# Kernel optimization log

Measured on AMD Instinct MI355X. Metric: run time of the kernel, lower is better.

Reference implementation:

```python
import jax, jax.numpy as jnp
import numpy as np

EMB = 384
H = 6
D = 64
B = 256
T = 256


def setup_inputs() -> dict:
    key = jax.random.key(0)
    ks = jax.random.split(key, 6)
    s = 1.0 / np.sqrt(EMB)
    return {
        "x": jax.random.normal(ks[0], (B, T, EMB), dtype=jnp.float32),
        "wq": jax.random.normal(ks[1], (H, EMB, D), dtype=jnp.float32) * s,
        "wk": jax.random.normal(ks[2], (H, EMB, D), dtype=jnp.float32) * s,
        "wv": jax.random.normal(ks[3], (H, EMB, D), dtype=jnp.float32) * s,
        "w_proj": jax.random.normal(ks[4], (H * D, EMB), dtype=jnp.float32) * s,
        "b_proj": jax.random.normal(ks[5], (EMB,), dtype=jnp.float32) * 0.01,
    }


def reference(x, wq, wk, wv, w_proj, b_proj):
    # x: [B, T, E]; per-head projections stacked over H (dropout in eval mode)
    q = jnp.einsum("bte,hed->bhtd", x, wq)
    k = jnp.einsum("bte,hed->bhtd", x, wk)
    v = jnp.einsum("bte,hed->bhtd", x, wv)
    scale = q.shape[-1] ** -0.5
    scores = jnp.einsum("bhqd,bhkd->bhqk", q, k) * scale  # [B,H,T,T]
    tq = q.shape[2]
    causal = jnp.tril(jnp.ones((tq, tq), dtype=bool))
    scores = jnp.where(causal, scores, -jnp.inf)
    att = jax.nn.softmax(scores, axis=-1)
    out = jnp.einsum("bhqk,bhkd->bhqd", att, v)  # [B,H,T,D]
    out = out.transpose(0, 2, 1, 3).reshape(x.shape[0], tq, -1)  # concat heads
    return out @ w_proj + b_proj
```

## Files before the change

kernel.cpp:

```cpp
#include <hip/hip_runtime.h>
#include <hip/hip_bf16.h>


#define Bn 256
#define Tn 256
#define En 384
#define Hn 6
#define Dn 64

typedef __bf16 bf16x8 __attribute__((ext_vector_type(8)));
typedef float f32x4 __attribute__((ext_vector_type(4)));
typedef unsigned short u16x8 __attribute__((ext_vector_type(8)));

static __device__ __forceinline__ unsigned short f2bf(float f) {
    unsigned int u = __builtin_bit_cast(unsigned int, f);
    u += 0x7fffu + ((u >> 16) & 1u);
    return (unsigned short)(u >> 16);
}

static __device__ __forceinline__ f32x4 mfma16(bf16x8 a, bf16x8 b, f32x4 c) {
    return __builtin_amdgcn_mfma_f32_16x16x32_bf16(a, b, c, 0, 0, 0);
}

static __device__ __forceinline__ void glds16(const unsigned short* g, unsigned short* l) {
    __builtin_amdgcn_global_load_lds(
        (const __attribute__((address_space(1))) unsigned int*)g,
        (__attribute__((address_space(3))) unsigned int*)l, 16, 0, 0);
}

__global__ __launch_bounds__(256) void prep_xcast_kernel(
    const float* __restrict__ wq, const float* __restrict__ wk,
    const float* __restrict__ wv, const float* __restrict__ wp,
    const float* __restrict__ x,
    unsigned short* __restrict__ wt, unsigned short* __restrict__ wpt,
    unsigned short* __restrict__ xb) {
    const int bid = blockIdx.x;
    if (bid < 12288) {
        size_t i = ((size_t)bid * 256 + threadIdx.x) * 8;
        float4 f0 = *(const float4*)(x + i);
        float4 f1 = *(const float4*)(x + i + 4);
        u16x8 p;
        p[0] = f2bf(f0.x); p[1] = f2bf(f0.y); p[2] = f2bf(f0.z); p[3] = f2bf(f0.w);
        p[4] = f2bf(f1.x); p[5] = f2bf(f1.y); p[6] = f2bf(f1.z); p[7] = f2bf(f1.w);
        *(u16x8*)(xb + i) = p;
    } else {
        const int NW = 3 * Hn * Dn * En;
        const int NP = En * En;
        int idx = (bid - 12288) * 256 + threadIdx.x;
        if (idx < NW) {
            int e = idx % En;
            int d = (idx / En) % Dn;
            int h = (idx / (En * Dn)) % Hn;
            int t = idx / (En * Dn * Hn);
            const float* src = (t == 0) ? wq : (t == 1) ? wk : wv;
            wt[idx] = f2bf(src[(h * En + e) * Dn + d]);
        } else if (idx < NW + NP) {
            int j = idx - NW;
            int k = j % En;
            int n = j / En;
            wpt[j] = f2bf(wp[k * En + n]);
        }
    }
}

__global__ __launch_bounds__(256) void qkv_gemm(
    const unsigned short* __restrict__ xb, const unsigned short* __restrict__ wt,
    unsigned short* __restrict__ Qo, unsigned short* __restrict__ Ko,
    unsigned short* __restrict__ Vt) {
    __shared__ unsigned short As[4][128][32];
    __shared__ unsigned short Bs[4][192][32];

    const int bid = blockIdx.x;
    const int swz = (bid & 7) * 384 + (bid >> 3);
    const int h = swz % Hn;
    const int m0 = (swz / Hn) * 128;

    const int tid = threadIdx.x;
    const int wave = tid >> 6, lane = tid & 63;
    const int quad = lane >> 4, l16 = lane & 15;
    const int mw = (wave >> 1) * 64, nw = (wave & 1) * 96;

    f32x4 acc[4][6];
#pragma unroll
    for (int i = 0; i < 4; ++i)
#pragma unroll
        for (int j = 0; j < 6; ++j) acc[i][j] = (f32x4){0.f, 0.f, 0.f, 0.f};

    const int lrow = lane >> 2;
    const int js = (lane & 3) ^ ((lane >> 3) & 3);

    const unsigned short* ga[2];
#pragma unroll
    for (int i = 0; i < 2; ++i)
        ga[i] = xb + (size_t)(m0 + wave * 32 + i * 16 + lrow) * En + js * 8;
    const unsigned short* gb[3];
#pragma unroll
    for (int i = 0; i < 3; ++i) {
        int n = wave * 48 + i * 16 + lrow;
        gb[i] = wt + (size_t)(((n >> 6) * Hn + h) * Dn + (n & 63)) * En + js * 8;
    }

#define QKV_STAGE(buf, koff)                                              \
    do {                                                                  \
        glds16(ga[0] + (koff), &As[buf][wave * 32][0]);                   \
        glds16(ga[1] + (koff), &As[buf][wave * 32 + 16][0]);              \
        glds16(gb[0] + (koff), &Bs[buf][wave * 48][0]);                   \
        glds16(gb[1] + (koff), &Bs[buf][wave * 48 + 16][0]);              \
        glds16(gb[2] + (koff), &Bs[buf][wave * 48 + 32][0]);              \
    } while (0)

    QKV_STAGE(0, 0);
    QKV_STAGE(1, 32);
    QKV_STAGE(2, 64);

    const int ps = (quad ^ ((l16 >> 1) & 3)) * 8;

#pragma unroll
    for (int kb = 0; kb < 12; ++kb) {
        if (kb <= 9)       asm volatile("s_waitcnt vmcnt(10)" ::: "memory");
        else if (kb == 10) asm volatile("s_waitcnt vmcnt(5)" ::: "memory");
        else               asm volatile("s_waitcnt vmcnt(0)" ::: "memory");
        __builtin_amdgcn_s_barrier();
        if (kb < 9) QKV_STAGE((kb + 3) & 3, (kb + 3) * 32);

        const int cur = kb & 3;
        bf16x8 a[4], b[6];
#pragma unroll
        for (int mi = 0; mi < 4; ++mi)
            a[mi] = *(const bf16x8*)&As[cur][mw + mi * 16 + l16][ps];
#pragma unroll
        for (int ni = 0; ni < 6; ++ni)
            b[ni] = *(const bf16x8*)&Bs[cur][nw + ni * 16 + l16][ps];
#pragma unroll
        for (int mi = 0; mi < 4; ++mi)
#pragma unroll
            for (int ni = 0; ni < 6; ++ni) acc[mi][ni] = mfma16(a[mi], b[ni], acc[mi][ni]);
    }
#undef QKV_STAGE

    const int b = m0 >> 8, tbase = m0 & 255;
    unsigned short* qkbase[2] = {
        Qo + (size_t)((b * Hn + h) * Tn) * Dn,
        Ko + (size_t)((b * Hn + h) * Tn) * Dn };
    unsigned short* vdst = Vt + (size_t)((b * Hn + h) * Dn) * Tn;
#pragma unroll
    for (int ni = 0; ni < 6; ++ni) {
        const int ng = nw + ni * 16;
        const int tensor = ng >> 6;
        const int d = (ng & 63) + l16;
        if (tensor < 2) {
            unsigned short* dst = qkbase[tensor];
#pragma unroll
            for (int mi = 0; mi < 4; ++mi)
#pragma unroll
                for (int r = 0; r < 4; ++r) {
                    int t = tbase + mw + mi * 16 + quad * 4 + r;
                    dst[t * Dn + d] = f2bf(acc[mi][ni][r]);
                }
        } else {
#pragma unroll
            for (int mi = 0; mi < 4; ++mi) {
                int t0 = tbase + mw + mi * 16 + quad * 4;
                ushort4 pk;
                pk.x = f2bf(acc[mi][ni][0]);
                pk.y = f2bf(acc[mi][ni][1]);
                pk.z = f2bf(acc[mi][ni][2]);
                pk.w = f2bf(acc[mi][ni][3]);
                *(ushort4*)&vdst[d * Tn + t0] = pk;
            }
        }
    }
}

__global__ __launch_bounds__(256) void attn_kernel(
    const unsigned short* __restrict__ Q, const unsigned short* __restrict__ K,
    const unsigned short* __restrict__ Vt, unsigned short* __restrict__ attout) {
    __shared__ unsigned short Kt[256][64];
    __shared__ unsigned short Vl[64][256];
    __shared__ unsigned short P[4][16][72];

    const int h = blockIdx.x, b = blockIdx.y;
    const unsigned short* Qb = Q + (size_t)((b * Hn + h) * Tn) * Dn;
    const unsigned short* Kb = K + (size_t)((b * Hn + h) * Tn) * Dn;
    const unsigned short* Vb = Vt + (size_t)((b * Hn + h) * Dn) * Tn;

    const int tid = threadIdx.x;
    const int wave = tid >> 6, lane = tid & 63;
    const int quad = lane >> 4, l16 = lane & 15;

    const int grp[4] = {wave, 7 - wave, 8 + wave, 15 - wave};

    {
        const unsigned short* kg = Kb + (size_t)(lane >> 3) * Dn + ((lane & 7) ^ (lane >> 3)) * 8;
#pragma unroll
        for (int i = 0; i < 8; ++i) {
            const int c = wave * 8 + i;
            glds16(kg + (size_t)c * 8 * Dn, &Kt[c * 8][0]);
        }
#pragma unroll
        for (int i = 0; i < 8; ++i) {
            const int c = wave * 8 + i;
            const int d = c * 2 + (lane >> 5);
            const int j = (lane & 31) ^ (d & 7);
            glds16(Vb + (size_t)d * Tn + j * 8, &Vl[c * 2][0]);
        }
    }

    bf16x8 aq[4][2];
#pragma unroll
    for (int gi = 0; gi < 4; ++gi) {
        const int q0 = grp[gi] * 16;
#pragma unroll
        for (int ks = 0; ks < 2; ++ks)
            aq[gi][ks] = *(const bf16x8*)&Qb[(q0 + l16) * Dn + ks * 32 + quad * 8];
    }

    __syncthreads();

    const float cexp = 0.125f * 1.44269504f;

#pragma unroll
    for (int gi = 0; gi < 4; ++gi) {
        const int g = grp[gi];
        const int q0 = g * 16;

        f32x4 O[4];
#pragma unroll
        for (int i = 0; i < 4; ++i) O[i] = (f32x4){0.f, 0.f, 0.f, 0.f};
        float rsum[4] = {0.f, 0.f, 0.f, 0.f};

        const int ktmax = g >> 2;
        for (int kt = 0; kt <= ktmax; ++kt) {
            f32x4 S[4];
#pragma unroll
            for (int i = 0; i < 4; ++i) S[i] = (f32x4){0.f, 0.f, 0.f, 0.f};
            __builtin_amdgcn_s_setprio(1);
#pragma unroll
            for (int ks = 0; ks < 2; ++ks)
#pragma unroll
                for (int ni = 0; ni < 4; ++ni) {
                    bf16x8 bk = *(const bf16x8*)
                        &Kt[kt * 64 + ni * 16 + l16][(((ks * 4 + quad) ^ (l16 & 7)) * 8)];
                    S[ni] = mfma16(aq[gi][ks], bk, S[ni]);
                }
            __builtin_amdgcn_s_setprio(0);

#pragma unroll
            for (int ni = 0; ni < 4; ++ni)
#pragma unroll
                for (int r = 0; r < 4; ++r) {
                    int col = kt * 64 + ni * 16 + l16;
                    float p = exp2f(S[ni][r] * cexp);
                    p = (col > q0 + quad * 4 + r) ? 0.f : p;
                    rsum[r] += p;
                    P[wave][quad * 4 + r][ni * 16 + l16] = f2bf(p);
                }

            __builtin_amdgcn_s_setprio(1);
#pragma unroll
            for (int ks = 0; ks < 2; ++ks) {
                bf16x8 ap = *(const bf16x8*)&P[wave][l16][ks * 32 + quad * 8];
#pragma unroll
                for (int ni = 0; ni < 4; ++ni) {
                    bf16x8 bv = *(const bf16x8*)
                        &Vl[ni * 16 + l16][(((kt * 8 + ks * 4 + quad) ^ (l16 & 7)) * 8)];
                    O[ni] = mfma16(ap, bv, O[ni]);
                }
            }
            __builtin_amdgcn_s_setprio(0);
        }

#pragma unroll
        for (int r = 0; r < 4; ++r) {
            float s = rsum[r];
            s += __shfl_xor(s, 1);
            s += __shfl_xor(s, 2);
            s += __shfl_xor(s, 4);
            s += __shfl_xor(s, 8);
            rsum[r] = s;
        }

#pragma unroll
        for (int r = 0; r < 4; ++r) {
            float inv = 1.0f / rsum[r];
#pragma unroll
            for (int ni = 0; ni < 4; ++ni)
                P[wave][quad * 4 + r][ni * 16 + l16] = f2bf(O[ni][r] * inv);
        }
        const int row = lane >> 2;
        const int colc = (lane & 3) * 16;
        unsigned short* dst = attout + (size_t)(b * Tn + q0 + row) * (Hn * Dn) + h * Dn + colc;
        *(uint4*)dst = *(const uint4*)&P[wave][row][colc];
        *(uint4*)(dst + 8) = *(const uint4*)&P[wave][row][colc + 8];
    }
}

__global__ __launch_bounds__(256) void proj_gemm(
    const unsigned short* __restrict__ attout, const unsigned short* __restrict__ wpt,
    const float* __restrict__ bproj, float* __restrict__ out) {
    __shared__ unsigned short As[2][128][64];
    __shared__ unsigned short Bs[2][128][64];

    const int bid = blockIdx.x;
    const int swz = (bid & 7) * 192 + (bid >> 3);
    const int n0 = (swz % 3) * 128;
    const int m0 = (swz / 3) * 128;

    const int tid = threadIdx.x;
    const int wave = tid >> 6, lane = tid & 63;
    const int quad = lane >> 4, l16 = lane & 15;
    const int mw = (wave >> 1) * 64, nw = (wave & 1) * 64;

    f32x4 acc[4][4];
#pragma unroll
    for (int i = 0; i < 4; ++i)
#pragma unroll
        for (int j = 0; j < 4; ++j) acc[i][j] = (f32x4){0.f, 0.f, 0.f, 0.f};

    const int lr = lane >> 3;
    const int js = (lane & 7) ^ lr;

    const unsigned short* ga[4];
    const unsigned short* gb[4];
#pragma unroll
    for (int i = 0; i < 4; ++i) {
        ga[i] = attout + (size_t)(m0 + wave * 32 + i * 8 + lr) * En + js * 8;
        gb[i] = wpt + (size_t)(n0 + wave * 32 + i * 8 + lr) * En + js * 8;
    }

#define PROJ_STAGE(buf, koff)                                             \
    do {                                                                  \
        _Pragma("unroll") for (int i = 0; i < 4; ++i)                     \
            glds16(ga[i] + (koff), &As[buf][wave * 32 + i * 8][0]);       \
        _Pragma("unroll") for (int i = 0; i < 4; ++i)                     \
            glds16(gb[i] + (koff), &Bs[buf][wave * 32 + i * 8][0]);       \
    } while (0)

    PROJ_STAGE(0, 0);
    PROJ_STAGE(1, 64);

#pragma unroll
    for (int kb = 0; kb < 6; ++kb) {
        if (kb < 5) asm volatile("s_waitcnt vmcnt(8)" ::: "memory");
        else        asm volatile("s_waitcnt vmcnt(0)" ::: "memory");
        __builtin_amdgcn_s_barrier();

        const int cur = kb & 1;
        __builtin_amdgcn_s_setprio(1);
#pragma unroll
        for (int ks = 0; ks < 2; ++ks) {
            bf16x8 a[4], bb[4];
            const int ps = ((ks * 4 + quad) ^ (l16 & 7)) * 8;
#pragma unroll
            for (int mi = 0; mi < 4; ++mi)
                a[mi] = *(const bf16x8*)&As[cur][mw + mi * 16 + l16][ps];
#pragma unroll
            for (int ni = 0; ni < 4; ++ni)
                bb[ni] = *(const bf16x8*)&Bs[cur][nw + ni * 16 + l16][ps];
#pragma unroll
            for (int mi = 0; mi < 4; ++mi)
#pragma unroll
                for (int ni = 0; ni < 4; ++ni) acc[mi][ni] = mfma16(a[mi], bb[ni], acc[mi][ni]);
        }
        __builtin_amdgcn_s_setprio(0);

        if (kb < 4) {
            __builtin_amdgcn_s_barrier();
            PROJ_STAGE(cur, (kb + 2) * 64);
        }
    }
#undef PROJ_STAGE

#pragma unroll
    for (int mi = 0; mi < 4; ++mi)
#pragma unroll
        for (int ni = 0; ni < 4; ++ni)
#pragma unroll
            for (int r = 0; r < 4; ++r) {
                int row = m0 + mw + mi * 16 + quad * 4 + r;
                int col = n0 + nw + ni * 16 + l16;
                out[(size_t)row * En + col] = acc[mi][ni][r] + bproj[col];
            }
}

extern "C" void kernel_launch(void* const* d_in, const int* in_sizes, int n_in,
                              void* d_out, int out_size, void* d_ws, size_t ws_size,
                              hipStream_t stream) {
    const float* x  = (const float*)d_in[0];
    const float* wq = (const float*)d_in[1];
    const float* wk = (const float*)d_in[2];
    const float* wv = (const float*)d_in[3];
    const float* wp = (const float*)d_in[4];
    const float* bp = (const float*)d_in[5];
    float* out = (float*)d_out;

    char* ws = (char*)d_ws;
    const size_t WT_OFF  = 0;
    const size_t WPT_OFF = WT_OFF + 884736;
    const size_t Q_OFF   = WPT_OFF + 294912;
    const size_t K_OFF   = Q_OFF + 50331648ull;
    const size_t VT_OFF  = K_OFF + 50331648ull;
    const size_t XB_OFF  = VT_OFF + 50331648ull;

    unsigned short* wt   = (unsigned short*)(ws + WT_OFF);
    unsigned short* wpt  = (unsigned short*)(ws + WPT_OFF);
    unsigned short* Qd   = (unsigned short*)(ws + Q_OFF);
    unsigned short* Kd   = (unsigned short*)(ws + K_OFF);
    unsigned short* Vtd  = (unsigned short*)(ws + VT_OFF);
    unsigned short* xbd  = (unsigned short*)(ws + XB_OFF);
    unsigned short* ao   = xbd;

    prep_xcast_kernel<<<14592, 256, 0, stream>>>(wq, wk, wv, wp, x, wt, wpt, xbd);
    qkv_gemm<<<3072, 256, 0, stream>>>(xbd, wt, Qd, Kd, Vtd);
    attn_kernel<<<dim3(Hn, Bn), 256, 0, stream>>>(Qd, Kd, Vtd, ao);
    proj_gemm<<<1536, 256, 0, stream>>>(ao, wpt, bp, out);
}
```

Baseline: 360.4 us.

## Fuse QKV projection GEMM into attention kernel, keeping Q/K/V in LDS

Merges the QKV GEMM and attention kernels so each block computes Q, K and V for one (batch, head) pair directly into shared memory and then runs causal attention on them. This removes the global-memory round trip for Q, K and V and one kernel launch. In exchange each block uses about 156KB of LDS, which limits occupancy to one block per CU, the grid shrinks, and the GEMM pipeline drops from four stages to three, so latency hiding is weaker.

```diff
diff --git a/kernel.cpp b/kernel.cpp
--- a/kernel.cpp
+++ b/kernel.cpp
@@ -63,17 +63,21 @@
     }
 }
 
-__global__ __launch_bounds__(256) void qkv_gemm(
+__global__ __launch_bounds__(256, 1) void qkvattn_kernel(
     const unsigned short* __restrict__ xb, const unsigned short* __restrict__ wt,
-    unsigned short* __restrict__ Qo, unsigned short* __restrict__ Ko,
-    unsigned short* __restrict__ Vt) {
-    __shared__ unsigned short As[4][128][32];
-    __shared__ unsigned short Bs[4][192][32];
+    unsigned short* __restrict__ attout) {
+    __shared__ __align__(16) unsigned short smem[79872];
+    unsigned short (*Kt)[64]      = (unsigned short(*)[64])(smem);
+    unsigned short (*Vl)[256]     = (unsigned short(*)[256])(smem + 16384);
+    unsigned short (*Qs)[64]      = (unsigned short(*)[64])(smem + 32768);
+    unsigned short (*As)[128][32] = (unsigned short(*)[128][32])(smem + 49152);
+    unsigned short (*Bs)[192][32] = (unsigned short(*)[192][32])(smem + 61440);
+    unsigned short (*P)[16][72]   = (unsigned short(*)[16][72])(smem + 49152);
 
     const int bid = blockIdx.x;
-    const int swz = (bid & 7) * 384 + (bid >> 3);
-    const int h = swz % Hn;
-    const int m0 = (swz / Hn) * 128;
+    const int swz = (bid & 7) * 192 + (bid >> 3);
+    const int bi = swz / Hn;
+    const int h  = swz % Hn;
 
     const int tid = threadIdx.x;
     const int wave = tid >> 6, lane = tid & 63;
@@ -92,7 +96,7 @@
     const unsigned short* ga[2];
 #pragma unroll
     for (int i = 0; i < 2; ++i)
-        ga[i] = xb + (size_t)(m0 + wave * 32 + i * 16 + lrow) * En + js * 8;
+        ga[i] = xb + (size_t)(bi * 256 + wave * 32 + i * 16 + lrow) * En + js * 8;
     const unsigned short* gb[3];
 #pragma unroll
     for (int i = 0; i < 3; ++i) {
@@ -100,130 +104,103 @@
         gb[i] = wt + (size_t)(((n >> 6) * Hn + h) * Dn + (n & 63)) * En + js * 8;
     }
 
-#define QKV_STAGE(buf, koff)                                              \
-    do {                                                                  \
-        glds16(ga[0] + (koff), &As[buf][wave * 32][0]);                   \
-        glds16(ga[1] + (koff), &As[buf][wave * 32 + 16][0]);              \
-        glds16(gb[0] + (koff), &Bs[buf][wave * 48][0]);                   \
-        glds16(gb[1] + (koff), &Bs[buf][wave * 48 + 16][0]);              \
-        glds16(gb[2] + (koff), &Bs[buf][wave * 48 + 32][0]);              \
+#define QA_STAGE(c)                                                          \
+    do {                                                                     \
+        const int _buf = (c) % 3;                                            \
+        const size_t _ao = (size_t)((c) / 12) * (128 * En) + ((c) % 12) * 32;\
+        const size_t _bo = (size_t)((c) % 12) * 32;                          \
+        glds16(ga[0] + _ao, &As[_buf][wave * 32][0]);                        \
+        glds16(ga[1] + _ao, &As[_buf][wave * 32 + 16][0]);                   \
+        glds16(gb[0] + _bo, &Bs[_buf][wave * 48][0]);                        \
+        glds16(gb[1] + _bo, &Bs[_buf][wave * 48 + 16][0]);                   \
+        glds16(gb[2] + _bo, &Bs[_buf][wave * 48 + 32][0]);                   \
     } while (0)
 
-    QKV_STAGE(0, 0);
-    QKV_STAGE(1, 32);
-    QKV_STAGE(2, 64);
+#define QA_EPI(half)                                                         \
+    do {                                                                     \
+        _Pragma("unroll") for (int ni = 0; ni < 6; ++ni) {                   \
+            const int ng = nw + ni * 16;                                     \
+            const int tensor = ng >> 6;                                      \
+            const int d = (ng & 63) + l16;                                   \
+            if (tensor == 2) {                                               \
+                _Pragma("unroll") for (int mi = 0; mi < 4; ++mi) {           \
+                    const int t0 = (half) * 128 + mw + mi * 16 + quad * 4;   \
+                    ushort4 pk;                                              \
+                    pk.x = f2bf(acc[mi][ni][0]);                             \
+                    pk.y = f2bf(acc[mi][ni][1]);                             \
+                    pk.z = f2bf(acc[mi][ni][2]);                             \
+                    pk.w = f2bf(acc[mi][ni][3]);                             \
+                    *(ushort4*)&Vl[d][((((t0 >> 3) ^ (d & 7))) << 3) + (t0 & 4)] = pk; \
+                }                                                            \
+            } else {                                                         \
+                unsigned short(*dstl)[64] = (tensor == 0) ? Qs : Kt;         \
+                _Pragma("unroll") for (int mi = 0; mi < 4; ++mi)             \
+                    _Pragma("unroll") for (int r = 0; r < 4; ++r) {          \
+                        const int t = (half) * 128 + mw + mi * 16 + quad * 4 + r; \
+                        dstl[t][((((d >> 3) ^ (t & 7))) << 3) + (d & 7)] =   \
+                            f2bf(acc[mi][ni][r]);                            \
+                    }                                                        \
+            }                                                                \
+        }                                                                    \
+    } while (0)
+
+    QA_STAGE(0);
+    QA_STAGE(1);
 
     const int ps = (quad ^ ((l16 >> 1) & 3)) * 8;
 
 #pragma unroll
-    for (int kb = 0; kb < 12; ++kb) {
-        if (kb <= 9)       asm volatile("s_waitcnt vmcnt(10)" ::: "memory");
-        else if (kb == 10) asm volatile("s_waitcnt vmcnt(5)" ::: "memory");
-        else               asm volatile("s_waitcnt vmcnt(0)" ::: "memory");
+    for (int k = 0; k < 24; ++k) {
         __builtin_amdgcn_s_barrier();
-        if (kb < 9) QKV_STAGE((kb + 3) & 3, (kb + 3) * 32);
-
-        const int cur = kb & 3;
-        bf16x8 a[4], b[6];
+        if (k < 22) {
+            QA_STAGE(k + 2);
+            asm volatile("s_waitcnt vmcnt(10)" ::: "memory");
+        } else if (k == 22) {
+            asm volatile("s_waitcnt vmcnt(5)" ::: "memory");
+        } else {
+            asm volatile("s_waitcnt vmcnt(0)" ::: "memory");
+        }
+
+        const int cur = k % 3;
+        bf16x8 a[4], bq[6];
 #pragma unroll
         for (int mi = 0; mi < 4; ++mi)
             a[mi] = *(const bf16x8*)&As[cur][mw + mi * 16 + l16][ps];
 #pragma unroll
         for (int ni = 0; ni < 6; ++ni)
-            b[ni] = *(const bf16x8*)&Bs[cur][nw + ni * 16 + l16][ps];
+            bq[ni] = *(const bf16x8*)&Bs[cur][nw + ni * 16 + l16][ps];
 #pragma unroll
         for (int mi = 0; mi < 4; ++mi)
 #pragma unroll
-            for (int ni = 0; ni < 6; ++ni) acc[mi][ni] = mfma16(a[mi], b[ni], acc[mi][ni]);
-    }
-#undef QKV_STAGE
-
-    const int b = m0 >> 8, tbase = m0 & 255;
-    unsigned short* qkbase[2] = {
-        Qo + (size_t)((b * Hn + h) * Tn) * Dn,
-        Ko + (size_t)((b * Hn + h) * Tn) * Dn };
-    unsigned short* vdst = Vt + (size_t)((b * Hn + h) * Dn) * Tn;
-#pragma unroll
-    for (int ni = 0; ni < 6; ++ni) {
-        const int ng = nw + ni * 16;
-        const int tensor = ng >> 6;
-        const int d = (ng & 63) + l16;
-        if (tensor < 2) {
-            unsigned short* dst = qkbase[tensor];
-#pragma unroll
-            for (int mi = 0; mi < 4; ++mi)
-#pragma unroll
-                for (int r = 0; r < 4; ++r) {
-                    int t = tbase + mw + mi * 16 + quad * 4 + r;
-                    dst[t * Dn + d] = f2bf(acc[mi][ni][r]);
-                }
-        } else {
-#pragma unroll
-            for (int mi = 0; mi < 4; ++mi) {
-                int t0 = tbase + mw + mi * 16 + quad * 4;
-                ushort4 pk;
-                pk.x = f2bf(acc[mi][ni][0]);
-                pk.y = f2bf(acc[mi][ni][1]);
-                pk.z = f2bf(acc[mi][ni][2]);
-                pk.w = f2bf(acc[mi][ni][3]);
-                *(ushort4*)&vdst[d * Tn + t0] = pk;
-            }
-        }
-    }
-}
-
-__global__ __launch_bounds__(256) void attn_kernel(
-    const unsigned short* __restrict__ Q, const unsigned short* __restrict__ K,
-    const unsigned short* __restrict__ Vt, unsigned short* __restrict__ attout) {
-    __shared__ unsigned short Kt[256][64];
-    __shared__ unsigned short Vl[64][256];
-    __shared__ unsigned short P[4][16][72];
-
-    const int h = blockIdx.x, b = blockIdx.y;
-    const unsigned short* Qb = Q + (size_t)((b * Hn + h) * Tn) * Dn;
-    const unsigned short* Kb = K + (size_t)((b * Hn + h) * Tn) * Dn;
-    const unsigned short* Vb = Vt + (size_t)((b * Hn + h) * Dn) * Tn;
-
-    const int tid = threadIdx.x;
-    const int wave = tid >> 6, lane = tid & 63;
-    const int quad = lane >> 4, l16 = lane & 15;
-
+            for (int ni = 0; ni < 6; ++ni) acc[mi][ni] = mfma16(a[mi], bq[ni], acc[mi][ni]);
+
+        if (k == 11) {
+            QA_EPI(0);
+#pragma unroll
+            for (int i = 0; i < 4; ++i)
+#pragma unroll
+                for (int j = 0; j < 6; ++j) acc[i][j] = (f32x4){0.f, 0.f, 0.f, 0.f};
+        }
+    }
+    QA_EPI(1);
+#undef QA_STAGE
+#undef QA_EPI
+
+    __syncthreads();
+
+    const float cexp = 0.125f * 1.44269504f;
     const int grp[4] = {wave, 7 - wave, 8 + wave, 15 - wave};
-
-    {
-        const unsigned short* kg = Kb + (size_t)(lane >> 3) * Dn + ((lane & 7) ^ (lane >> 3)) * 8;
-#pragma unroll
-        for (int i = 0; i < 8; ++i) {
-            const int c = wave * 8 + i;
-            glds16(kg + (size_t)c * 8 * Dn, &Kt[c * 8][0]);
-        }
-#pragma unroll
-        for (int i = 0; i < 8; ++i) {
-            const int c = wave * 8 + i;
-            const int d = c * 2 + (lane >> 5);
-            const int j = (lane & 31) ^ (d & 7);
-            glds16(Vb + (size_t)d * Tn + j * 8, &Vl[c * 2][0]);
-        }
-    }
-
-    bf16x8 aq[4][2];
-#pragma unroll
-    for (int gi = 0; gi < 4; ++gi) {
-        const int q0 = grp[gi] * 16;
-#pragma unroll
-        for (int ks = 0; ks < 2; ++ks)
-            aq[gi][ks] = *(const bf16x8*)&Qb[(q0 + l16) * Dn + ks * 32 + quad * 8];
-    }
-
-    __syncthreads();
-
-    const float cexp = 0.125f * 1.44269504f;
 
 #pragma unroll
     for (int gi = 0; gi < 4; ++gi) {
         const int g = grp[gi];
         const int q0 = g * 16;
 
+        bf16x8 aq[2];
+#pragma unroll
+        for (int ks = 0; ks < 2; ++ks)
+            aq[ks] = *(const bf16x8*)&Qs[q0 + l16][(((ks * 4 + quad) ^ (l16 & 7)) * 8)];
+
         f32x4 O[4];
 #pragma unroll
         for (int i = 0; i < 4; ++i) O[i] = (f32x4){0.f, 0.f, 0.f, 0.f};
@@ -241,7 +218,7 @@
                 for (int ni = 0; ni < 4; ++ni) {
                     bf16x8 bk = *(const bf16x8*)
                         &Kt[kt * 64 + ni * 16 + l16][(((ks * 4 + quad) ^ (l16 & 7)) * 8)];
-                    S[ni] = mfma16(aq[gi][ks], bk, S[ni]);
+                    S[ni] = mfma16(aq[ks], bk, S[ni]);
                 }
             __builtin_amdgcn_s_setprio(0);
 
@@ -289,7 +266,7 @@
         }
         const int row = lane >> 2;
         const int colc = (lane & 3) * 16;
-        unsigned short* dst = attout + (size_t)(b * Tn + q0 + row) * (Hn * Dn) + h * Dn + colc;
+        unsigned short* dst = attout + (size_t)(bi * Tn + q0 + row) * (Hn * Dn) + h * Dn + colc;
         *(uint4*)dst = *(const uint4*)&P[wave][row][colc];
         *(uint4*)(dst + 8) = *(const uint4*)&P[wave][row][colc + 8];
     }
@@ -397,21 +374,15 @@
     char* ws = (char*)d_ws;
     const size_t WT_OFF  = 0;
     const size_t WPT_OFF = WT_OFF + 884736;
-    const size_t Q_OFF   = WPT_OFF + 294912;
-    const size_t K_OFF   = Q_OFF + 50331648ull;
-    const size_t VT_OFF  = K_OFF + 50331648ull;
-    const size_t XB_OFF  = VT_OFF + 50331648ull;
+    const size_t AO_OFF  = WPT_OFF + 294912;
+    const size_t XB_OFF  = AO_OFF + 50331648ull;
 
     unsigned short* wt   = (unsigned short*)(ws + WT_OFF);
     unsigned short* wpt  = (unsigned short*)(ws + WPT_OFF);
-    unsigned short* Qd   = (unsigned short*)(ws + Q_OFF);
-    unsigned short* Kd   = (unsigned short*)(ws + K_OFF);
-    unsigned short* Vtd  = (unsigned short*)(ws + VT_OFF);
+    unsigned short* ao   = (unsigned short*)(ws + AO_OFF);
     unsigned short* xbd  = (unsigned short*)(ws + XB_OFF);
-    unsigned short* ao   = xbd;
 
     prep_xcast_kernel<<<14592, 256, 0, stream>>>(wq, wk, wv, wp, x, wt, wpt, xbd);
-    qkv_gemm<<<3072, 256, 0, stream>>>(xbd, wt, Qd, Kd, Vtd);
-    attn_kernel<<<dim3(Hn, Bn), 256, 0, stream>>>(Qd, Kd, Vtd, ao);
+    qkvattn_kernel<<<1536, 256, 0, stream>>>(xbd, wt, ao);
     proj_gemm<<<1536, 256, 0, stream>>>(ao, wpt, bp, out);
 }
```

New measurement: 354.9 us. Within noise of the previous version (-1.5%).
